# Kernel tuning notes

Measured on AMD Instinct MI355X. Metric: run time of the kernel, lower is better.

## Reference

```python
import jax, jax.numpy as jnp
import numpy as np

B, GRID, C, K = 8, 24, 768, 3          # batch, ViT patch grid, embed dim, PatchMaker patchsize
PRE_DIM, TGT_DIM = 1024, 1024          # pretrain_embed_dimension, target_embed_dimension
N_MEM, IMG = 20000, 384                # coreset memory bank size, input image size


def adaptive_avg_pool_matrix(lin, lout):
    """Dense matrix M (lout, lin) so that x @ M.T == F.adaptive_avg_pool1d(x, lout)."""
    M = np.zeros((lout, lin), dtype=np.float32)
    for i in range(lout):
        s = (i * lin) // lout
        e = -(((-(i + 1)) * lin) // lout)  # ceil((i+1)*lin/lout)
        M[i, s:e] = 1.0 / (e - s)
    return jnp.asarray(M)


def unfold3x3(x):
    """torch.nn.Unfold(kernel=3, stride=1, pad=1): (B,C,H,W) -> (B, H*W, C, 3, 3)."""
    b, c, h, w = x.shape
    xp = jnp.pad(x, ((0, 0), (0, 0), (1, 1), (1, 1)))
    # stack shifted views in torch Unfold's (C, kh, kw) channel-major order
    p = jnp.stack([xp[:, :, i:i + h, j:j + w] for i in range(K) for j in range(K)], axis=2)
    p = p.reshape(b, c, K, K, h * w).transpose(0, 4, 1, 2, 3)
    return p


def setup_inputs() -> dict:
    key = jax.random.key(0)
    k1, k2, k3, k4 = jax.random.split(key, 4)
    return {
        "feats6": jax.random.normal(k1, (B, GRID * GRID + 1, C), jnp.float32),
        "feats8": jax.random.normal(k2, (B, GRID * GRID + 1, C), jnp.float32),
        "feats10": jax.random.normal(k3, (B, GRID * GRID + 1, C), jnp.float32),
        "memory_bank": jax.random.normal(k4, (N_MEM, TGT_DIM), jnp.float32),
    }


def reference(feats6, feats8, feats10, memory_bank):
    Mpre = adaptive_avg_pool_matrix(C * K * K, PRE_DIM)   # MeanMapper pooling
    Magg = adaptive_avg_pool_matrix(3 * PRE_DIM, TGT_DIM)  # Aggregator pooling

    pooled = []
    for f in (feats6, feats8, feats10):
        # drop CLS token, reshape to CNN-like grid (B, C, 24, 24)
        g = f[:, 1:, :].reshape(B, GRID, GRID, C).transpose(0, 3, 1, 2)
        # patchify (all layers share the 24x24 grid, so the bilinear re-alignment
        # to ref_num_patches in the original code is an identity here)
        p = unfold3x3(g).reshape(B * GRID * GRID, C * K * K)
        pooled.append(p @ Mpre.T)                         # (N, PRE_DIM)
    feats = jnp.stack(pooled, axis=1).reshape(-1, 3 * PRE_DIM)
    emb = feats @ Magg.T                                  # (N, TGT_DIM)

    # squared-L2 nearest neighbour against coreset memory bank (FaissNN IndexFlatL2)
    d2 = (jnp.sum(emb * emb, axis=1, keepdims=True)
          + jnp.sum(memory_bank * memory_bank, axis=1)[None, :]
          - 2.0 * emb @ memory_bank.T)                    # (N, N_MEM)
    patch_scores = jnp.min(d2, axis=1)                    # anomaly_score_num_nn = 1

    ps = patch_scores.reshape(B, GRID, GRID)
    image_scores = jnp.max(ps.reshape(B, -1), axis=1)     # PatchMaker.score (max over patches)
    masks = jax.image.resize(ps, (B, IMG, IMG), method="bilinear")  # RescaleSegmentor
    return image_scores, masks
```

## Files before the change

kernel.cpp:

```cpp
#include <hip/hip_runtime.h>
#include <hip/hip_bf16.h>
#include <stdint.h>

#define B_      8
#define GRID_   24
#define C_      768
#define NPATCH  (B_*GRID_*GRID_)
#define PRE     1024
#define TGT     1024
#define NMEM    20000
#define NMEM_PAD 20224
#define IMG_    384
#define SEQ     577

typedef __bf16 bf16_t;
typedef bf16_t bf16x8 __attribute__((ext_vector_type(8)));
typedef bf16_t bf16x4 __attribute__((ext_vector_type(4)));
typedef float  floatx4 __attribute__((ext_vector_type(4)));

__global__ __launch_bounds__(256) void emb_kernel(
    const float* __restrict__ f6, const float* __restrict__ f8,
    const float* __restrict__ f10,
    bf16_t* __restrict__ emb, float* __restrict__ enorm)
{
    __shared__ float pooled[3*PRE];
    __shared__ float red[4];

    const int n   = blockIdx.x;
    const int b   = n / (GRID_*GRID_);
    const int yx  = n - b*(GRID_*GRID_);
    const int y   = yx / GRID_;
    const int x   = yx - y*GRID_;
    const int t   = threadIdx.x;

    const float* fl[3] = {f6, f8, f10};

#pragma unroll
    for (int l = 0; l < 3; ++l) {
        const float* f = fl[l];
        float A0 = 0.f, B0 = 0.f, C1 = 0.f, D1 = 0.f, E2 = 0.f, F2 = 0.f;
#pragma unroll
        for (int k = 0; k < 9; ++k) {
            const int kh = k / 3, kw = k - kh*3;
            const int ny = y + kh - 1, nx = x + kw - 1;
            const bool v = (ny >= 0 && ny < GRID_ && nx >= 0 && nx < GRID_);
            const int off = v ? (b*SEQ + 1 + ny*GRID_ + nx) : (b*SEQ);
            const float* p = f + (size_t)off*C_ + 3*t;
            float a = p[0], bq = p[1], c = p[2];
            if (!v) { a = 0.f; bq = 0.f; c = 0.f; }
            if (k <= 6) A0 += a;
            if (k >= 6) B0 += a;
            if (k <= 4) C1 += bq;
            if (k >= 4) D1 += bq;
            if (k <= 2) E2 += c;
            if (k >= 2) F2 += c;
        }
        float4 pv;
        pv.x = A0 * (1.f/7.f);
        pv.y = (B0 + C1) * (1.f/8.f);
        pv.z = (D1 + E2) * (1.f/8.f);
        pv.w = F2 * (1.f/7.f);
        *(float4*)(pooled + l*PRE + 4*t) = pv;
    }
    __syncthreads();

    float psq = 0.f;
    bf16x4 ev;
#pragma unroll
    for (int r = 0; r < 4; ++r) {
        const int j = 4*t + r;
        float vv = (pooled[3*j] + pooled[3*j+1] + pooled[3*j+2]) * (1.f/3.f);
        ev[r] = (bf16_t)vv;
        psq += vv*vv;
    }
    *(bf16x4*)(emb + (size_t)n*TGT + 4*t) = ev;

    for (int off = 32; off > 0; off >>= 1) psq += __shfl_down(psq, off, 64);
    if ((t & 63) == 0) red[t >> 6] = psq;
    __syncthreads();
    if (t == 0) enorm[n] = (red[0] + red[1]) + (red[2] + red[3]);
}

__global__ __launch_bounds__(256) void mprep_kernel(
    const float* __restrict__ mb, bf16_t* __restrict__ mbf,
    float* __restrict__ mnorm)
{
    const int r = blockIdx.x;
    const int t = threadIdx.x;
    __shared__ float red[4];
    float psq = 0.f;
    if (r < NMEM) {
        float4 v = ((const float4*)(mb + (size_t)r*TGT))[t];
        bf16x4 o;
        o[0] = (bf16_t)v.x; o[1] = (bf16_t)v.y;
        o[2] = (bf16_t)v.z; o[3] = (bf16_t)v.w;
        ((bf16x4*)(mbf + (size_t)r*TGT))[t] = o;
        psq = v.x*v.x + v.y*v.y + v.z*v.z + v.w*v.w;
    } else {
        bf16x4 z; z[0] = z[1] = z[2] = z[3] = (bf16_t)0.f;
        ((bf16x4*)(mbf + (size_t)r*TGT))[t] = z;
    }
    for (int off = 32; off > 0; off >>= 1) psq += __shfl_down(psq, off, 64);
    if ((t & 63) == 0) red[t >> 6] = psq;
    __syncthreads();
    if (t == 0) mnorm[r] = (r < NMEM) ? ((red[0]+red[1])+(red[2]+red[3])) : 1e30f;
}

__global__ void init_kernel(int* __restrict__ p)
{
    int i = blockIdx.x*256 + threadIdx.x;
    if (i < NPATCH) p[i] = 0x7f7f7f7f;
}

__device__ __forceinline__ void load_lds16(const void* g, void* l)
{
    __builtin_amdgcn_global_load_lds(
        (__attribute__((address_space(1))) void*)g,
        (__attribute__((address_space(3))) void*)l, 16, 0, 0);
}

#define BAR()   do { asm volatile("" ::: "memory"); \
                     __builtin_amdgcn_s_barrier(); \
                     asm volatile("" ::: "memory"); } while (0)
#define LGKM0() asm volatile("s_waitcnt lgkmcnt(0)" ::: "memory")
#define VM4()   asm volatile("s_waitcnt vmcnt(4)" ::: "memory")

__global__ __launch_bounds__(512, 2) void nnmin_kernel(
    const bf16_t* __restrict__ E, const bf16_t* __restrict__ M,
    const float* __restrict__ enorm, const float* __restrict__ mnorm,
    int* __restrict__ out_min)
{
    __shared__ __attribute__((aligned(16))) bf16_t SA[2][256*64];
    __shared__ __attribute__((aligned(16))) bf16_t SB[2][256*64];

    const int m0   = blockIdx.x * 256;
    const int n0   = blockIdx.y * 256;
    const int tid  = threadIdx.x;
    const int lane = tid & 63;
    const int wave = tid >> 6;
    const int wm   = wave >> 2;
    const int wn   = wave & 3;
    const int fr   = lane & 15;
    const int fg   = lane >> 4;

    const int grow = tid >> 3;
    const int gks  = (tid & 7) ^ (grow & 7);
    const int lofs = tid * 8;

    const bf16_t* pA = E + (size_t)(m0 + grow)*TGT + gks*8;
    const bf16_t* pB = M + (size_t)(n0 + grow)*TGT + gks*8;

    const int xs0  = (fg)     ^ (fr & 7);
    const int xs1  = (4 + fg) ^ (fr & 7);
    const int arow = (wm*128 + fr) * 64;
    const int brow = (wn*64  + fr) * 64;

    floatx4 acc[8][4];
#pragma unroll
    for (int i = 0; i < 8; ++i)
#pragma unroll
        for (int j = 0; j < 4; ++j) acc[i][j] = (floatx4)0.0f;

#define STG_A(buf, tk, j) load_lds16(pA + (size_t)(j)*64*TGT + (tk)*64, \
                                     &SA[buf][(j)*4096 + lofs])
#define STG_B(buf, tk, j) load_lds16(pB + (size_t)(j)*64*TGT + (tk)*64, \
                                     &SB[buf][(j)*4096 + lofs])

#define RD_A(buf, mh, A_) do { \
    _Pragma("unroll") \
    for (int _m = 0; _m < 4; ++_m) { \
        A_[_m][0] = *(const bf16x8*)&SA[buf][arow + ((mh)*4+_m)*1024 + xs0*8]; \
        A_[_m][1] = *(const bf16x8*)&SA[buf][arow + ((mh)*4+_m)*1024 + xs1*8]; } } while (0)

#define RD_B(buf, nh, B_) do { \
    _Pragma("unroll") \
    for (int _n = 0; _n < 2; ++_n) { \
        B_[_n][0] = *(const bf16x8*)&SB[buf][brow + ((nh)*2+_n)*1024 + xs0*8]; \
        B_[_n][1] = *(const bf16x8*)&SB[buf][brow + ((nh)*2+_n)*1024 + xs1*8]; } } while (0)

#define MFMA16(mh, nh, A_, B_) do { \
    __builtin_amdgcn_s_setprio(1); \
    _Pragma("unroll") \
    for (int _m = 0; _m < 4; ++_m) \
    _Pragma("unroll") \
    for (int _n = 0; _n < 2; ++_n) { \
        acc[(mh)*4+_m][(nh)*2+_n] = __builtin_amdgcn_mfma_f32_16x16x32_bf16( \
            A_[_m][0], B_[_n][0], acc[(mh)*4+_m][(nh)*2+_n], 0, 0, 0); \
        acc[(mh)*4+_m][(nh)*2+_n] = __builtin_amdgcn_mfma_f32_16x16x32_bf16( \
            A_[_m][1], B_[_n][1], acc[(mh)*4+_m][(nh)*2+_n], 0, 0, 0); } \
    __builtin_amdgcn_s_setprio(0); } while (0)

#define TILE(bufc, bufn, tkA, tkB) do { \
    RD_A(bufc, 0, aa); RD_B(bufc, 0, bb); \
    STG_A(bufn, tkA, 0); STG_A(bufn, tkA, 1); \
    BAR(); LGKM0(); MFMA16(0, 0, aa, bb); BAR(); \
    RD_B(bufc, 1, bc); \
    STG_A(bufn, tkA, 2); STG_A(bufn, tkA, 3); \
    BAR(); LGKM0(); MFMA16(0, 1, aa, bc); BAR(); \
    RD_A(bufc, 1, aa); \
    STG_B(bufc, tkB, 0); STG_B(bufc, tkB, 1); \
    BAR(); LGKM0(); MFMA16(1, 0, aa, bb); BAR(); \
    STG_B(bufc, tkB, 2); STG_B(bufc, tkB, 3); \
    VM4(); BAR(); MFMA16(1, 1, aa, bc); BAR(); \
} while (0)

    bf16x8 aa[4][2], bb[2][2], bc[2][2];

#pragma unroll
    for (int j = 0; j < 4; ++j) STG_A(0, 0, j);
#pragma unroll
    for (int j = 0; j < 4; ++j) STG_B(0, 0, j);
#pragma unroll
    for (int j = 0; j < 4; ++j) STG_B(1, 1, j);
    VM4(); BAR();

    for (int t = 0; t < 16; t += 2) {
        const int a0 = t + 1;
        const int b0 = (t + 2 < 16) ? t + 2 : 15;
        TILE(0, 1, a0, b0);
        const int a1 = (t + 2 < 16) ? t + 2 : 15;
        const int b1 = (t + 3 < 16) ? t + 3 : 15;
        TILE(1, 0, a1, b1);
    }

#undef STG_A
#undef STG_B
#undef RD_A
#undef RD_B
#undef MFMA16
#undef TILE

    float mn[4];
#pragma unroll
    for (int tn = 0; tn < 4; ++tn)
        mn[tn] = mnorm[n0 + wn*64 + tn*16 + fr];
    const int rowq = fg * 4;
#pragma unroll
    for (int tm = 0; tm < 8; ++tm) {
#pragma unroll
        for (int r = 0; r < 4; ++r) {
            const int row = m0 + wm*128 + tm*16 + rowq + r;
            const float en = enorm[row];
            float best = 1e38f;
#pragma unroll
            for (int tn = 0; tn < 4; ++tn)
                best = fminf(best, en + mn[tn] - 2.0f*acc[tm][tn][r]);
#pragma unroll
            for (int off = 1; off < 16; off <<= 1)
                best = fminf(best, __shfl_xor(best, off, 64));
            if (fr == 0)
                atomicMin(&out_min[row], __float_as_int(best));
        }
    }
}

__global__ __launch_bounds__(256) void score_kernel(
    const int* __restrict__ ps_bits, float* __restrict__ out)
{
    const int b = blockIdx.x, tid = threadIdx.x;
    __shared__ float red[4];
    float m = -1e38f;
    for (int i = tid; i < GRID_*GRID_; i += 256)
        m = fmaxf(m, __int_as_float(ps_bits[b*GRID_*GRID_ + i]));
    for (int off = 32; off > 0; off >>= 1) m = fmaxf(m, __shfl_down(m, off, 64));
    if ((tid & 63) == 0) red[tid >> 6] = m;
    __syncthreads();
    if (tid == 0) out[b] = fmaxf(fmaxf(red[0], red[1]), fmaxf(red[2], red[3]));
}

__global__ __launch_bounds__(256) void mask_kernel(
    const int* __restrict__ ps_bits, float* __restrict__ masks)
{
    int idx = blockIdx.x*256 + threadIdx.x;
    int b  = idx / (IMG_*IMG_);
    int p  = idx - b*(IMG_*IMG_);
    int oy = p / IMG_, ox = p - oy*IMG_;

    float fy = (oy + 0.5f) * (1.0f/16.0f) - 0.5f;
    float fx = (ox + 0.5f) * (1.0f/16.0f) - 0.5f;
    int y0 = (int)floorf(fy); float ty = fy - (float)y0;
    int x0 = (int)floorf(fx); float tx = fx - (float)x0;
    int y0c = min(max(y0, 0), GRID_-1), y1c = min(max(y0+1, 0), GRID_-1);
    int x0c = min(max(x0, 0), GRID_-1), x1c = min(max(x0+1, 0), GRID_-1);

    const int* psb = ps_bits + b*GRID_*GRID_;
    float v00 = __int_as_float(psb[y0c*GRID_ + x0c]);
    float v01 = __int_as_float(psb[y0c*GRID_ + x1c]);
    float v10 = __int_as_float(psb[y1c*GRID_ + x0c]);
    float v11 = __int_as_float(psb[y1c*GRID_ + x1c]);
    float v0 = v00 + (v01 - v00)*tx;
    float v1 = v10 + (v11 - v10)*tx;
    masks[idx] = v0 + (v1 - v0)*ty;
}

extern "C" void kernel_launch(void* const* d_in, const int* in_sizes, int n_in,
                              void* d_out, int out_size, void* d_ws, size_t ws_size,
                              hipStream_t stream)
{
    const float* f6  = (const float*)d_in[0];
    const float* f8  = (const float*)d_in[1];
    const float* f10 = (const float*)d_in[2];
    const float* mb  = (const float*)d_in[3];
    float* out = (float*)d_out;

    char* ws = (char*)d_ws;
    bf16_t* emb  = (bf16_t*)ws;  ws += (size_t)NPATCH*TGT*sizeof(bf16_t);
    bf16_t* mbf  = (bf16_t*)ws;  ws += (size_t)NMEM_PAD*TGT*sizeof(bf16_t);
    float* enorm = (float*)ws;   ws += (size_t)NPATCH*sizeof(float);
    float* mnorm = (float*)ws;   ws += (size_t)NMEM_PAD*sizeof(float);
    int* psbits  = (int*)ws;     ws += (size_t)NPATCH*sizeof(int);

    hipLaunchKernelGGL(emb_kernel, dim3(NPATCH), dim3(256), 0, stream,
                       f6, f8, f10, emb, enorm);
    hipLaunchKernelGGL(mprep_kernel, dim3(NMEM_PAD), dim3(256), 0, stream,
                       mb, mbf, mnorm);
    hipLaunchKernelGGL(init_kernel, dim3((NPATCH+255)/256), dim3(256), 0, stream,
                       psbits);
    hipLaunchKernelGGL(nnmin_kernel, dim3(NPATCH/256, NMEM_PAD/256), dim3(512),
                       0, stream, emb, mbf, enorm, mnorm, psbits);
    hipLaunchKernelGGL(score_kernel, dim3(B_), dim3(256), 0, stream,
                       psbits, out);
    hipLaunchKernelGGL(mask_kernel, dim3((B_*IMG_*IMG_)/256), dim3(256), 0, stream,
                       psbits, out + B_);
}
```

Baseline: 429.6 us.

## Fuse prep kernels, merge score/mask kernels, remap GEMM blocks across XCDs

Merges the embedding, memory-bank conversion and min-buffer init into one launch, with memory rows handled one per wave. Score and mask kernels are merged into a single finishing kernel. The NN-min GEMM grid is remapped so consecutive tiles land on the same XCD, improving L2 reuse of shared A/B tiles. This cuts launch count and inter-kernel gaps, at the cost of a more heterogeneous prep kernel.

```diff
diff --git a/kernel.cpp b/kernel.cpp
--- a/kernel.cpp
+++ b/kernel.cpp
@@ -12,26 +12,62 @@
 #define NMEM_PAD 20224
 #define IMG_    384
 #define SEQ     577
+#define GM      (NPATCH/256)
+#define GN      (NMEM_PAD/256)
 
 typedef __bf16 bf16_t;
 typedef bf16_t bf16x8 __attribute__((ext_vector_type(8)));
 typedef bf16_t bf16x4 __attribute__((ext_vector_type(4)));
 typedef float  floatx4 __attribute__((ext_vector_type(4)));
 
-__global__ __launch_bounds__(256) void emb_kernel(
+__global__ __launch_bounds__(256) void prep_kernel(
     const float* __restrict__ f6, const float* __restrict__ f8,
-    const float* __restrict__ f10,
-    bf16_t* __restrict__ emb, float* __restrict__ enorm)
+    const float* __restrict__ f10, const float* __restrict__ mb,
+    bf16_t* __restrict__ emb, float* __restrict__ enorm,
+    bf16_t* __restrict__ mbf, float* __restrict__ mnorm,
+    int* __restrict__ psbits)
 {
     __shared__ float pooled[3*PRE];
     __shared__ float red[4];
+
+    const int t = threadIdx.x;
+
+    if (blockIdx.x >= NPATCH) {
+        const int rbase = (blockIdx.x - NPATCH) * 4;
+        const int w     = t >> 6;
+        const int lane  = t & 63;
+        const int row   = rbase + w;
+        float psq = 0.f;
+        if (row < NMEM) {
+            const float4* src = (const float4*)(mb + (size_t)row*TGT);
+            bf16x4*       dst = (bf16x4*)(mbf + (size_t)row*TGT);
+#pragma unroll
+            for (int j = 0; j < 4; ++j) {
+                float4 v = src[j*64 + lane];
+                bf16x4 o;
+                o[0] = (bf16_t)v.x; o[1] = (bf16_t)v.y;
+                o[2] = (bf16_t)v.z; o[3] = (bf16_t)v.w;
+                dst[j*64 + lane] = o;
+                psq += v.x*v.x + v.y*v.y + v.z*v.z + v.w*v.w;
+            }
+        } else {
+            bf16x4 z; z[0] = z[1] = z[2] = z[3] = (bf16_t)0.f;
+            bf16x4* dst = (bf16x4*)(mbf + (size_t)row*TGT);
+#pragma unroll
+            for (int j = 0; j < 4; ++j) dst[j*64 + lane] = z;
+        }
+        for (int off = 32; off > 0; off >>= 1) psq += __shfl_down(psq, off, 64);
+        if (lane == 0) mnorm[row] = (row < NMEM) ? psq : 1e30f;
+        return;
+    }
 
     const int n   = blockIdx.x;
     const int b   = n / (GRID_*GRID_);
     const int yx  = n - b*(GRID_*GRID_);
     const int y   = yx / GRID_;
     const int x   = yx - y*GRID_;
-    const int t   = threadIdx.x;
+
+    if (t == 0) psbits[n] = 0x7f7f7f7f;
 
     const float* fl[3] = {f6, f8, f10};
 
@@ -81,37 +117,6 @@
     if (t == 0) enorm[n] = (red[0] + red[1]) + (red[2] + red[3]);
 }
 
-__global__ __launch_bounds__(256) void mprep_kernel(
-    const float* __restrict__ mb, bf16_t* __restrict__ mbf,
-    float* __restrict__ mnorm)
-{
-    const int r = blockIdx.x;
-    const int t = threadIdx.x;
-    __shared__ float red[4];
-    float psq = 0.f;
-    if (r < NMEM) {
-        float4 v = ((const float4*)(mb + (size_t)r*TGT))[t];
-        bf16x4 o;
-        o[0] = (bf16_t)v.x; o[1] = (bf16_t)v.y;
-        o[2] = (bf16_t)v.z; o[3] = (bf16_t)v.w;
-        ((bf16x4*)(mbf + (size_t)r*TGT))[t] = o;
-        psq = v.x*v.x + v.y*v.y + v.z*v.z + v.w*v.w;
-    } else {
-        bf16x4 z; z[0] = z[1] = z[2] = z[3] = (bf16_t)0.f;
-        ((bf16x4*)(mbf + (size_t)r*TGT))[t] = z;
-    }
-    for (int off = 32; off > 0; off >>= 1) psq += __shfl_down(psq, off, 64);
-    if ((t & 63) == 0) red[t >> 6] = psq;
-    __syncthreads();
-    if (t == 0) mnorm[r] = (r < NMEM) ? ((red[0]+red[1])+(red[2]+red[3])) : 1e30f;
-}
-
-__global__ void init_kernel(int* __restrict__ p)
-{
-    int i = blockIdx.x*256 + threadIdx.x;
-    if (i < NPATCH) p[i] = 0x7f7f7f7f;
-}
-
 __device__ __forceinline__ void load_lds16(const void* g, void* l)
 {
     __builtin_amdgcn_global_load_lds(
@@ -133,8 +138,15 @@
     __shared__ __attribute__((aligned(16))) bf16_t SA[2][256*64];
     __shared__ __attribute__((aligned(16))) bf16_t SB[2][256*64];
 
-    const int m0   = blockIdx.x * 256;
-    const int n0   = blockIdx.y * 256;
+    const int orig = blockIdx.y * GM + blockIdx.x;
+    const int q    = (GM*GN) >> 3;
+    const int r    = (GM*GN) & 7;
+    const int xcd  = orig & 7;
+    const int pos  = orig >> 3;
+    const int nid  = (xcd < r ? xcd*(q+1) : r*(q+1) + (xcd - r)*q) + pos;
+    const int m0   = (nid % GM) * 256;
+    const int n0   = (nid / GM) * 256;
+
     const int tid  = threadIdx.x;
     const int lane = tid & 63;
     const int wave = tid >> 6;
@@ -254,27 +266,16 @@
     }
 }
 
-__global__ __launch_bounds__(256) void score_kernel(
-    const int* __restrict__ ps_bits, float* __restrict__ out)
-{
-    const int b = blockIdx.x, tid = threadIdx.x;
+__global__ __launch_bounds__(256) void finish_kernel(
+    const int* __restrict__ ps_bits, float* __restrict__ scores,
+    float* __restrict__ masks)
+{
     __shared__ float red[4];
-    float m = -1e38f;
-    for (int i = tid; i < GRID_*GRID_; i += 256)
-        m = fmaxf(m, __int_as_float(ps_bits[b*GRID_*GRID_ + i]));
-    for (int off = 32; off > 0; off >>= 1) m = fmaxf(m, __shfl_down(m, off, 64));
-    if ((tid & 63) == 0) red[tid >> 6] = m;
-    __syncthreads();
-    if (tid == 0) out[b] = fmaxf(fmaxf(red[0], red[1]), fmaxf(red[2], red[3]));
-}
-
-__global__ __launch_bounds__(256) void mask_kernel(
-    const int* __restrict__ ps_bits, float* __restrict__ masks)
-{
-    int idx = blockIdx.x*256 + threadIdx.x;
-    int b  = idx / (IMG_*IMG_);
-    int p  = idx - b*(IMG_*IMG_);
-    int oy = p / IMG_, ox = p - oy*IMG_;
+    const int tid = threadIdx.x;
+    const int idx = blockIdx.x*256 + tid;
+    const int b   = idx / (IMG_*IMG_);
+    const int p   = idx - b*(IMG_*IMG_);
+    const int oy  = p / IMG_, ox = p - oy*IMG_;
 
     float fy = (oy + 0.5f) * (1.0f/16.0f) - 0.5f;
     float fx = (ox + 0.5f) * (1.0f/16.0f) - 0.5f;
@@ -291,6 +292,18 @@
     float v0 = v00 + (v01 - v00)*tx;
     float v1 = v10 + (v11 - v10)*tx;
     masks[idx] = v0 + (v1 - v0)*ty;
+
+    if (blockIdx.x < B_) {
+        const int sb = blockIdx.x;
+        float m = -1e38f;
+        for (int i = tid; i < GRID_*GRID_; i += 256)
+            m = fmaxf(m, __int_as_float(ps_bits[sb*GRID_*GRID_ + i]));
+        for (int off = 32; off > 0; off >>= 1) m = fmaxf(m, __shfl_down(m, off, 64));
+        if ((tid & 63) == 0) red[tid >> 6] = m;
+        __syncthreads();
+        if (tid == 0)
+            scores[sb] = fmaxf(fmaxf(red[0], red[1]), fmaxf(red[2], red[3]));
+    }
 }
 
 extern "C" void kernel_launch(void* const* d_in, const int* in_sizes, int n_in,
@@ -310,16 +323,10 @@
     float* mnorm = (float*)ws;   ws += (size_t)NMEM_PAD*sizeof(float);
     int* psbits  = (int*)ws;     ws += (size_t)NPATCH*sizeof(int);
 
-    hipLaunchKernelGGL(emb_kernel, dim3(NPATCH), dim3(256), 0, stream,
-                       f6, f8, f10, emb, enorm);
-    hipLaunchKernelGGL(mprep_kernel, dim3(NMEM_PAD), dim3(256), 0, stream,
-                       mb, mbf, mnorm);
-    hipLaunchKernelGGL(init_kernel, dim3((NPATCH+255)/256), dim3(256), 0, stream,
-                       psbits);
-    hipLaunchKernelGGL(nnmin_kernel, dim3(NPATCH/256, NMEM_PAD/256), dim3(512),
+    hipLaunchKernelGGL(prep_kernel, dim3(NPATCH + NMEM_PAD/4), dim3(256), 0, stream,
+                       f6, f8, f10, mb, emb, enorm, mbf, mnorm, psbits);
+    hipLaunchKernelGGL(nnmin_kernel, dim3(GM, GN), dim3(512),
                        0, stream, emb, mbf, enorm, mnorm, psbits);
-    hipLaunchKernelGGL(score_kernel, dim3(B_), dim3(256), 0, stream,
-                       psbits, out);
-    hipLaunchKernelGGL(mask_kernel, dim3((B_*IMG_*IMG_)/256), dim3(256), 0, stream,
-                       psbits, out + B_);
-}
+    hipLaunchKernelGGL(finish_kernel, dim3((B_*IMG_*IMG_)/256), dim3(256), 0, stream,
+                       psbits, out, out + B_);
+}
```

New measurement: 419.7 us. 2.3% less time.
